# Performance work log

Hardware: AMD Instinct MI355X
Metric: run time of the kernel (lower is better)

The kernel has to match this reference:

```python
import jax, jax.numpy as jnp
import numpy as np

B, N, L = 1, 128, 256
D_MSA, D_HID, D_PAIR = 256, 32, 128
EPS = 1e-5


def setup_inputs() -> dict:
    key = jax.random.key(0)
    ks = jax.random.split(key, 8)
    msa = jax.random.normal(ks[0], (B, N, L, D_MSA), dtype=jnp.float32)
    pair = jax.random.normal(ks[1], (B, L, L, D_PAIR), dtype=jnp.float32)
    symmids = jax.random.randint(ks[2], (1,), 0, 1, dtype=jnp.int64)
    symmsub = jax.random.randint(ks[3], (1,), 0, 1, dtype=jnp.int64)
    # learned params (lecun-normal-ish scale = 1/sqrt(fan_in))
    ln_gamma = jnp.ones((D_MSA,), jnp.float32)
    ln_beta = jnp.zeros((D_MSA,), jnp.float32)
    w_left = jax.random.normal(ks[4], (D_MSA, D_HID), jnp.float32) / np.sqrt(D_MSA)
    b_left = jnp.zeros((D_HID,), jnp.float32)
    w_right = jax.random.normal(ks[5], (D_MSA, D_HID), jnp.float32) / np.sqrt(D_MSA)
    b_right = jnp.zeros((D_HID,), jnp.float32)
    w_out = jax.random.normal(ks[6], (D_HID * D_HID, D_PAIR), jnp.float32) / np.sqrt(D_HID * D_HID)
    b_out = jnp.zeros((D_PAIR,), jnp.float32)
    return {
        "msa": msa, "pair": pair, "symmids": symmids, "symmsub": symmsub,
        "ln_gamma": ln_gamma, "ln_beta": ln_beta,
        "w_left": w_left, "b_left": b_left,
        "w_right": w_right, "b_right": b_right,
        "w_out": w_out, "b_out": b_out,
    }


def reference(msa, pair, symmids, symmsub, ln_gamma, ln_beta,
              w_left, b_left, w_right, b_right, w_out, b_out):
    b, n, l, _ = msa.shape
    # LayerNorm over d_msa (biased variance, matching torch)
    mu = jnp.mean(msa, axis=-1, keepdims=True)
    var = jnp.mean(jnp.square(msa - mu), axis=-1, keepdims=True)
    x = (msa - mu) * jax.lax.rsqrt(var + EPS) * ln_gamma + ln_beta
    left = x @ w_left + b_left                       # [b, n, l, d_h]
    right = (x @ w_right + b_right) / float(n)       # [b, n, l, d_h]
    # outer product, reduced over MSA (s) dim -> [b, l, m, d_h, d_h]
    out = jnp.einsum('bsli,bsmj->blmij', left, right).reshape(b, l, l, -1)
    out = out @ w_out + b_out                        # [b, l, l, d_pair]
    return pair + out
```

## Files before the change

### kernel.cpp

```cpp
#include <hip/hip_runtime.h>


typedef float v4f __attribute__((ext_vector_type(4)));
typedef short v8s __attribute__((ext_vector_type(8)));

static __device__ inline unsigned short f2bf(float x) {
    unsigned int u = __builtin_bit_cast(unsigned int, x);
    return (unsigned short)((u + 0x7fffu + ((u >> 16) & 1u)) >> 16);
}

static __device__ inline void gl_lds16(const unsigned short* g, unsigned short* l) {
    __builtin_amdgcn_global_load_lds(
        (const __attribute__((address_space(1))) unsigned int*)g,
        (__attribute__((address_space(3))) unsigned int*)(unsigned long long)l,
        16, 0, 0);
}

__global__ __launch_bounds__(256) void k_prep(const float* __restrict__ w_out,
                                              const float* __restrict__ wl,
                                              const float* __restrict__ wr,
                                              unsigned short* __restrict__ w3,
                                              unsigned short* __restrict__ wB) {
    const int b = blockIdx.x, t = threadIdx.x;
    unsigned short tmp[8];
    if (b < 64) {
        int tgt = b * 2048 + t * 8;
        int lane6 = (tgt >> 3) & 63, quad = lane6 >> 4, l15 = lane6 & 15;
        int w = (tgt >> 9) & 3, tt = (tgt >> 11) & 1;
        int inner = (tgt >> 12) & 1, ck = tgt >> 13;
        int p = w * 32 + tt * 16 + l15;
        for (int e = 0; e < 8; ++e) {
            int kp = ck * 64 + inner * 32 + quad * 8 + e;
            int j1 = (kp >> 9) & 1, qd = (kp >> 7) & 3, lp = (kp >> 3) & 15;
            int i1 = (kp >> 2) & 1, r = kp & 3;
            int ii = i1 * 16 + qd * 4 + r, jj = j1 * 16 + lp;
            tmp[e] = f2bf(w_out[(ii * 32 + jj) * 128 + p]);
        }
        *(uint4*)&w3[tgt] = *(const uint4*)tmp;
    } else {
        int tgt = (b - 64) * 2048 + t * 8;
        int frag = tgt >> 9, lane6 = (tgt >> 3) & 63;
        int nt = frag >> 3, ks = frag & 7;
        int quad = lane6 >> 4, l15 = lane6 & 15;
        int c = nt * 16 + l15;
        const float* src = (c < 32) ? wl : wr;
        int cc = c & 31;
        for (int e = 0; e < 8; ++e) {
            int d = ks * 32 + quad * 8 + e;
            tmp[e] = f2bf(src[d * 32 + cc]);
        }
        *(uint4*)&wB[tgt] = *(const uint4*)tmp;
    }
}

__global__ __launch_bounds__(256) void k_lnproj(
    const float* __restrict__ msa, const float* __restrict__ gamma, const float* __restrict__ beta,
    const unsigned short* __restrict__ wB, const float* __restrict__ bl, const float* __restrict__ br,
    unsigned short* __restrict__ leftT, unsigned short* __restrict__ rightT) {
    __shared__ unsigned short xb[32 * 264];
    __shared__ unsigned short outT[64 * 40];

    const int t = threadIdx.x, lane = t & 63, w = t >> 6;
    const int l = blockIdx.x, s0 = blockIdx.y * 32;
    const int quad = lane >> 4, l15 = lane & 15;

    float4 g4 = *(const float4*)&gamma[lane * 4];
    float4 be4 = *(const float4*)&beta[lane * 4];
    float4 vr[8]; float s1[8], s2[8];
    for (int r = 0; r < 8; ++r) {
        const float* row = msa + (size_t)((s0 + w * 8 + r) * 256 + l) * 256;
        vr[r] = *(const float4*)&row[lane * 4];
    }
    for (int r = 0; r < 8; ++r) {
        float4 v = vr[r];
        s1[r] = v.x + v.y + v.z + v.w;
        s2[r] = v.x * v.x + v.y * v.y + v.z * v.z + v.w * v.w;
    }
    for (int o = 32; o > 0; o >>= 1)
        for (int r = 0; r < 8; ++r) { s1[r] += __shfl_xor(s1[r], o); s2[r] += __shfl_xor(s2[r], o); }
    for (int r = 0; r < 8; ++r) {
        float mu = s1[r] * (1.f / 256);
        float rs = rsqrtf(s2[r] * (1.f / 256) - mu * mu + 1e-5f);
        float4 v = vr[r];
        ushort4 xs;
        xs.x = f2bf((v.x - mu) * rs * g4.x + be4.x);
        xs.y = f2bf((v.y - mu) * rs * g4.y + be4.y);
        xs.z = f2bf((v.z - mu) * rs * g4.z + be4.z);
        xs.w = f2bf((v.w - mu) * rs * g4.w + be4.w);
        *(ushort4*)&xb[(w * 8 + r) * 264 + lane * 4] = xs;
    }
    __syncthreads();

    const int mt = w >> 1, ntb = (w & 1) * 2;
    v4f acc[2] = {};
    const int frow = (mt * 16 + l15) * 264;
    const unsigned short* wBp = wB + lane * 8;
#pragma unroll
    for (int ks = 0; ks < 8; ++ks) {
        v8s a = *(const v8s*)&xb[frow + ks * 32 + quad * 8];
        v8s b0 = *(const v8s*)&wBp[(ntb * 8 + ks) * 512];
        v8s b1 = *(const v8s*)&wBp[((ntb + 1) * 8 + ks) * 512];
        acc[0] = __builtin_amdgcn_mfma_f32_16x16x32_bf16(a, b0, acc[0], 0, 0, 0);
        acc[1] = __builtin_amdgcn_mfma_f32_16x16x32_bf16(a, b1, acc[1], 0, 0, 0);
    }

    for (int tn = 0; tn < 2; ++tn) {
        int c = (ntb + tn) * 16 + l15;
        float bias = c < 32 ? bl[c] : br[c - 32];
        float scale = c < 32 ? 1.f : (1.f / 128);
        for (int r = 0; r < 4; ++r)
            outT[c * 40 + mt * 16 + quad * 4 + r] = f2bf((acc[tn][r] + bias) * scale);
    }
    __syncthreads();

    {
        int c = t >> 2, q = t & 3;
        uint4 vv = *(const uint4*)&outT[c * 40 + q * 8];
        int cc = c & 31;
        unsigned short* base = (c < 32) ? leftT : rightT;
        unsigned short* dst = base + l * 4096 + blockIdx.y * 1024
                            + (cc >> 4) * 512 + q * 128 + (cc & 15) * 8;
        *(uint4*)dst = vv;
    }
}

__global__ __launch_bounds__(256, 3) void k_outer(
    const unsigned short* __restrict__ leftT, const unsigned short* __restrict__ rightT,
    const unsigned short* __restrict__ w2g, const float* __restrict__ bout,
    const float* __restrict__ pairIn, float* __restrict__ out) {
    __shared__ alignas(16) unsigned short smem[16384];
    unsigned short* Ah = smem;
    unsigned short* Bh = smem + 8192;
    unsigned short* Obuf = smem;

    const int t = threadIdx.x, lane = t & 63, w = t >> 6;
    const int l0 = blockIdx.x * 4, m0 = blockIdx.y * 4;
    const int wm = w & 1, wn = w >> 1;
    const int quad = lane >> 4, l15 = lane & 15;

    float pf[8];
#pragma unroll
    for (int tt = 0; tt < 2; ++tt)
#pragma unroll
        for (int r = 0; r < 4; ++r) {
            int pr = quad * 4 + r;
            int p = (w * 2 + tt) * 16 + l15;
            size_t idx = (size_t)((l0 + (pr >> 2)) * 256 + (m0 + (pr & 3))) * 128 + p;
            pf[tt * 4 + r] = pairIn[idx];
        }

    const unsigned short* Asrc = leftT + l0 * 4096;
    const unsigned short* Bsrc = rightT + m0 * 4096;

    v4f acc[4][4] = {};
    for (int kh = 0; kh < 2; ++kh) {
        if (kh) __syncthreads();
#pragma unroll
        for (int it = 0; it < 4; ++it) {
            int x = (it * 256 + t) * 8;
            gl_lds16(&Asrc[(x >> 11) * 4096 + kh * 2048 + (x & 2047)], &Ah[x]);
            gl_lds16(&Bsrc[(x >> 11) * 4096 + kh * 2048 + (x & 2047)], &Bh[x]);
        }
        __syncthreads();
#pragma unroll
        for (int kl = 0; kl < 2; ++kl) {
            v8s a[4], bb[4];
#pragma unroll
            for (int i = 0; i < 4; ++i)
                a[i] = *(const v8s*)&Ah[(wm * 2 + (i >> 1)) * 2048 + kl * 1024 + (i & 1) * 512 + lane * 8];
#pragma unroll
            for (int j = 0; j < 4; ++j)
                bb[j] = *(const v8s*)&Bh[(wn * 2 + (j >> 1)) * 2048 + kl * 1024 + (j & 1) * 512 + lane * 8];
#pragma unroll
            for (int i = 0; i < 4; ++i)
#pragma unroll
                for (int j = 0; j < 4; ++j)
                    acc[i][j] = __builtin_amdgcn_mfma_f32_16x16x32_bf16(a[i], bb[j], acc[i][j], 0, 0, 0);
        }
    }
    __syncthreads();

    const unsigned short* wsrc = w2g + w * 512 + lane * 8;
    v8s A0 = *(const v8s*)&wsrc[0];
    v8s A1 = *(const v8s*)&wsrc[2048];
    v8s A2 = *(const v8s*)&wsrc[4096];
    v8s A3 = *(const v8s*)&wsrc[6144];
    v8s B0 = *(const v8s*)&wsrc[8192];
    v8s B1 = *(const v8s*)&wsrc[8192 + 2048];
    v8s B2 = *(const v8s*)&wsrc[8192 + 4096];
    v8s B3 = *(const v8s*)&wsrc[8192 + 6144];

    for (int a2 = 0; a2 < 2; ++a2)
        for (int b2 = 0; b2 < 2; ++b2) {
            int P = (wm * 2 + a2) * 4 + wn * 2 + b2;
            for (int j1 = 0; j1 < 2; ++j1) {
                unsigned short tmp8[8];
                for (int i1 = 0; i1 < 2; ++i1)
                    for (int r = 0; r < 4; ++r)
                        tmp8[i1 * 4 + r] = f2bf(acc[a2 * 2 + i1][b2 * 2 + j1][r]);
                int pg = (j1 * 64 + lane) ^ (P & 7) ^ ((P & 8) << 3);
                *(uint4*)&Obuf[P * 1024 + pg * 8] = *(const uint4*)tmp8;
            }
        }
    __syncthreads();

    v4f aI0[2] = {}, aI1[2] = {};
#pragma unroll
    for (int ck = 0; ck < 16; ck += 2) {
        {
            int g = ck * 8 + quad;
            v8s a = *(const v8s*)&Obuf[l15 * 1024 + ((g ^ (l15 & 7) ^ ((l15 & 8) << 3)) << 3)];
            aI0[0] = __builtin_amdgcn_mfma_f32_16x16x32_bf16(a, A0, aI0[0], 0, 0, 0);
            aI0[1] = __builtin_amdgcn_mfma_f32_16x16x32_bf16(a, A1, aI0[1], 0, 0, 0);
            int g2 = ck * 8 + 4 + quad;
            v8s a2 = *(const v8s*)&Obuf[l15 * 1024 + ((g2 ^ (l15 & 7) ^ ((l15 & 8) << 3)) << 3)];
            aI1[0] = __builtin_amdgcn_mfma_f32_16x16x32_bf16(a2, A2, aI1[0], 0, 0, 0);
            aI1[1] = __builtin_amdgcn_mfma_f32_16x16x32_bf16(a2, A3, aI1[1], 0, 0, 0);
            if (ck + 2 < 16) {
                const unsigned short* nx = wsrc + (ck + 2) * 8192;
                A0 = *(const v8s*)&nx[0];
                A1 = *(const v8s*)&nx[2048];
                A2 = *(const v8s*)&nx[4096];
                A3 = *(const v8s*)&nx[6144];
            }
        }
        {
            int g = (ck + 1) * 8 + quad;
            v8s a = *(const v8s*)&Obuf[l15 * 1024 + ((g ^ (l15 & 7) ^ ((l15 & 8) << 3)) << 3)];
            aI0[0] = __builtin_amdgcn_mfma_f32_16x16x32_bf16(a, B0, aI0[0], 0, 0, 0);
            aI0[1] = __builtin_amdgcn_mfma_f32_16x16x32_bf16(a, B1, aI0[1], 0, 0, 0);
            int g2 = (ck + 1) * 8 + 4 + quad;
            v8s a2 = *(const v8s*)&Obuf[l15 * 1024 + ((g2 ^ (l15 & 7) ^ ((l15 & 8) << 3)) << 3)];
            aI1[0] = __builtin_amdgcn_mfma_f32_16x16x32_bf16(a2, B2, aI1[0], 0, 0, 0);
            aI1[1] = __builtin_amdgcn_mfma_f32_16x16x32_bf16(a2, B3, aI1[1], 0, 0, 0);
            if (ck + 3 < 16) {
                const unsigned short* nx = wsrc + (ck + 3) * 8192;
                B0 = *(const v8s*)&nx[0];
                B1 = *(const v8s*)&nx[2048];
                B2 = *(const v8s*)&nx[4096];
                B3 = *(const v8s*)&nx[6144];
            }
        }
    }

#pragma unroll
    for (int tt = 0; tt < 2; ++tt) {
        int p = (w * 2 + tt) * 16 + l15;
        float bo = bout[p];
        v4f acc2 = aI0[tt] + aI1[tt];
#pragma unroll
        for (int r = 0; r < 4; ++r) {
            int pr = quad * 4 + r;
            size_t idx = (size_t)((l0 + (pr >> 2)) * 256 + (m0 + (pr & 3))) * 128 + p;
            out[idx] = pf[tt * 4 + r] + bo + acc2[r];
        }
    }
}

extern "C" void kernel_launch(void* const* d_in, const int* in_sizes, int n_in,
                              void* d_out, int out_size, void* d_ws, size_t ws_size,
                              hipStream_t stream) {
    const float* msa   = (const float*)d_in[0];
    const float* pairI = (const float*)d_in[1];
    const float* gamma = (const float*)d_in[4];
    const float* beta  = (const float*)d_in[5];
    const float* wl    = (const float*)d_in[6];
    const float* bl    = (const float*)d_in[7];
    const float* wr    = (const float*)d_in[8];
    const float* br    = (const float*)d_in[9];
    const float* wout  = (const float*)d_in[10];
    const float* bout  = (const float*)d_in[11];
    float* out = (float*)d_out;

    unsigned short* leftT  = (unsigned short*)d_ws;
    unsigned short* rightT = leftT + 256 * 32 * 128;
    unsigned short* w3     = rightT + 256 * 32 * 128;
    unsigned short* wB     = w3 + 131072;

    k_prep<<<dim3(72), 256, 0, stream>>>(wout, wl, wr, w3, wB);
    k_lnproj<<<dim3(256, 4), 256, 0, stream>>>(msa, gamma, beta, wB, bl, br, leftT, rightT);
    k_outer<<<dim3(64, 64), 256, 0, stream>>>(leftT, rightT, w3, bout, pairI, out);
}
```

Before: 172.2 us.

## Enlarge outer-product tile to 8x4 pairs with 512-thread blocks

The k_outer block now covers 8 l rows by 4 m columns with 8 waves instead of 4x4 with 4 waves. Each wave owns 16 output channels and reuses every w_out fragment across two 16-pair row groups, which halves the per-block weight loads per output and lets the right operand be shared by more rows. The w_out pre-layout in k_prep is changed to match the new wave-to-channel mapping. The pair input prefetch also moves later, after the first GEMM. The cost is doubled LDS per block (64 KB) and a bigger register budget, which may reduce occupancy.

After: 178.3 us. +3.5%, slower.

```diff
diff --git a/kernel.cpp b/kernel.cpp
--- a/kernel.cpp
+++ b/kernel.cpp
@@ -26,9 +26,9 @@
     if (b < 64) {
         int tgt = b * 2048 + t * 8;
         int lane6 = (tgt >> 3) & 63, quad = lane6 >> 4, l15 = lane6 & 15;
-        int w = (tgt >> 9) & 3, tt = (tgt >> 11) & 1;
+        int w = (tgt >> 9) & 7;
         int inner = (tgt >> 12) & 1, ck = tgt >> 13;
-        int p = w * 32 + tt * 16 + l15;
+        int p = w * 16 + l15;
         for (int e = 0; e < 8; ++e) {
             int kp = ck * 64 + inner * 32 + quad * 8 + e;
             int j1 = (kp >> 9) & 1, qd = (kp >> 7) & 3, lp = (kp >> 3) & 15;
@@ -124,30 +124,19 @@
     }
 }
 
-__global__ __launch_bounds__(256, 3) void k_outer(
+__global__ __launch_bounds__(512, 4) void k_outer(
     const unsigned short* __restrict__ leftT, const unsigned short* __restrict__ rightT,
     const unsigned short* __restrict__ w2g, const float* __restrict__ bout,
     const float* __restrict__ pairIn, float* __restrict__ out) {
-    __shared__ alignas(16) unsigned short smem[16384];
+    __shared__ alignas(16) unsigned short smem[32768];
     unsigned short* Ah = smem;
-    unsigned short* Bh = smem + 8192;
+    unsigned short* Bh = smem + 16384;
     unsigned short* Obuf = smem;
 
     const int t = threadIdx.x, lane = t & 63, w = t >> 6;
-    const int l0 = blockIdx.x * 4, m0 = blockIdx.y * 4;
-    const int wm = w & 1, wn = w >> 1;
+    const int l0 = blockIdx.x * 8, m0 = blockIdx.y * 4;
+    const int wm = w & 3, wn = w >> 2;
     const int quad = lane >> 4, l15 = lane & 15;
-
-    float pf[8];
-#pragma unroll
-    for (int tt = 0; tt < 2; ++tt)
-#pragma unroll
-        for (int r = 0; r < 4; ++r) {
-            int pr = quad * 4 + r;
-            int p = (w * 2 + tt) * 16 + l15;
-            size_t idx = (size_t)((l0 + (pr >> 2)) * 256 + (m0 + (pr & 3))) * 128 + p;
-            pf[tt * 4 + r] = pairIn[idx];
-        }
 
     const unsigned short* Asrc = leftT + l0 * 4096;
     const unsigned short* Bsrc = rightT + m0 * 4096;
@@ -157,8 +146,12 @@
         if (kh) __syncthreads();
 #pragma unroll
         for (int it = 0; it < 4; ++it) {
-            int x = (it * 256 + t) * 8;
+            int x = (it * 512 + t) * 8;
             gl_lds16(&Asrc[(x >> 11) * 4096 + kh * 2048 + (x & 2047)], &Ah[x]);
+        }
+#pragma unroll
+        for (int it = 0; it < 2; ++it) {
+            int x = (it * 512 + t) * 8;
             gl_lds16(&Bsrc[(x >> 11) * 4096 + kh * 2048 + (x & 2047)], &Bh[x]);
         }
         __syncthreads();
@@ -182,13 +175,19 @@
 
     const unsigned short* wsrc = w2g + w * 512 + lane * 8;
     v8s A0 = *(const v8s*)&wsrc[0];
-    v8s A1 = *(const v8s*)&wsrc[2048];
-    v8s A2 = *(const v8s*)&wsrc[4096];
-    v8s A3 = *(const v8s*)&wsrc[6144];
+    v8s A1 = *(const v8s*)&wsrc[4096];
     v8s B0 = *(const v8s*)&wsrc[8192];
-    v8s B1 = *(const v8s*)&wsrc[8192 + 2048];
-    v8s B2 = *(const v8s*)&wsrc[8192 + 4096];
-    v8s B3 = *(const v8s*)&wsrc[8192 + 6144];
+    v8s B1 = *(const v8s*)&wsrc[8192 + 4096];
+    const int p = w * 16 + l15;
+    float bo = bout[p];
+    float pf[8];
+#pragma unroll
+    for (int pm = 0; pm < 2; ++pm)
+#pragma unroll
+        for (int r = 0; r < 4; ++r) {
+            int P = pm * 16 + quad * 4 + r;
+            pf[pm * 4 + r] = pairIn[(size_t)((l0 + (P >> 2)) * 256 + (m0 + (P & 3))) * 128 + p];
+        }
 
     for (int a2 = 0; a2 < 2; ++a2)
         for (int b2 = 0; b2 < 2; ++b2) {
@@ -209,52 +208,52 @@
     for (int ck = 0; ck < 16; ck += 2) {
         {
             int g = ck * 8 + quad;
-            v8s a = *(const v8s*)&Obuf[l15 * 1024 + ((g ^ (l15 & 7) ^ ((l15 & 8) << 3)) << 3)];
-            aI0[0] = __builtin_amdgcn_mfma_f32_16x16x32_bf16(a, A0, aI0[0], 0, 0, 0);
-            aI0[1] = __builtin_amdgcn_mfma_f32_16x16x32_bf16(a, A1, aI0[1], 0, 0, 0);
+            int ch = ((g ^ (l15 & 7) ^ ((l15 & 8) << 3)) << 3);
+            v8s a0 = *(const v8s*)&Obuf[l15 * 1024 + ch];
+            v8s a1 = *(const v8s*)&Obuf[(16 + l15) * 1024 + ch];
+            aI0[0] = __builtin_amdgcn_mfma_f32_16x16x32_bf16(a0, A0, aI0[0], 0, 0, 0);
+            aI0[1] = __builtin_amdgcn_mfma_f32_16x16x32_bf16(a1, A0, aI0[1], 0, 0, 0);
             int g2 = ck * 8 + 4 + quad;
-            v8s a2 = *(const v8s*)&Obuf[l15 * 1024 + ((g2 ^ (l15 & 7) ^ ((l15 & 8) << 3)) << 3)];
-            aI1[0] = __builtin_amdgcn_mfma_f32_16x16x32_bf16(a2, A2, aI1[0], 0, 0, 0);
-            aI1[1] = __builtin_amdgcn_mfma_f32_16x16x32_bf16(a2, A3, aI1[1], 0, 0, 0);
+            int ch2 = ((g2 ^ (l15 & 7) ^ ((l15 & 8) << 3)) << 3);
+            v8s b0 = *(const v8s*)&Obuf[l15 * 1024 + ch2];
+            v8s b1 = *(const v8s*)&Obuf[(16 + l15) * 1024 + ch2];
+            aI1[0] = __builtin_amdgcn_mfma_f32_16x16x32_bf16(b0, A1, aI1[0], 0, 0, 0);
+            aI1[1] = __builtin_amdgcn_mfma_f32_16x16x32_bf16(b1, A1, aI1[1], 0, 0, 0);
             if (ck + 2 < 16) {
                 const unsigned short* nx = wsrc + (ck + 2) * 8192;
                 A0 = *(const v8s*)&nx[0];
-                A1 = *(const v8s*)&nx[2048];
-                A2 = *(const v8s*)&nx[4096];
-                A3 = *(const v8s*)&nx[6144];
+                A1 = *(const v8s*)&nx[4096];
             }
         }
         {
             int g = (ck + 1) * 8 + quad;
-            v8s a = *(const v8s*)&Obuf[l15 * 1024 + ((g ^ (l15 & 7) ^ ((l15 & 8) << 3)) << 3)];
-            aI0[0] = __builtin_amdgcn_mfma_f32_16x16x32_bf16(a, B0, aI0[0], 0, 0, 0);
-            aI0[1] = __builtin_amdgcn_mfma_f32_16x16x32_bf16(a, B1, aI0[1], 0, 0, 0);
+            int ch = ((g ^ (l15 & 7) ^ ((l15 & 8) << 3)) << 3);
+            v8s a0 = *(const v8s*)&Obuf[l15 * 1024 + ch];
+            v8s a1 = *(const v8s*)&Obuf[(16 + l15) * 1024 + ch];
+            aI0[0] = __builtin_amdgcn_mfma_f32_16x16x32_bf16(a0, B0, aI0[0], 0, 0, 0);
+            aI0[1] = __builtin_amdgcn_mfma_f32_16x16x32_bf16(a1, B0, aI0[1], 0, 0, 0);
             int g2 = (ck + 1) * 8 + 4 + quad;
-            v8s a2 = *(const v8s*)&Obuf[l15 * 1024 + ((g2 ^ (l15 & 7) ^ ((l15 & 8) << 3)) << 3)];
-            aI1[0] = __builtin_amdgcn_mfma_f32_16x16x32_bf16(a2, B2, aI1[0], 0, 0, 0);
-            aI1[1] = __builtin_amdgcn_mfma_f32_16x16x32_bf16(a2, B3, aI1[1], 0, 0, 0);
+            int ch2 = ((g2 ^ (l15 & 7) ^ ((l15 & 8) << 3)) << 3);
+            v8s b0 = *(const v8s*)&Obuf[l15 * 1024 + ch2];
+            v8s b1 = *(const v8s*)&Obuf[(16 + l15) * 1024 + ch2];
+            aI1[0] = __builtin_amdgcn_mfma_f32_16x16x32_bf16(b0, B1, aI1[0], 0, 0, 0);
+            aI1[1] = __builtin_amdgcn_mfma_f32_16x16x32_bf16(b1, B1, aI1[1], 0, 0, 0);
             if (ck + 3 < 16) {
                 const unsigned short* nx = wsrc + (ck + 3) * 8192;
                 B0 = *(const v8s*)&nx[0];
-                B1 = *(const v8s*)&nx[2048];
-                B2 = *(const v8s*)&nx[4096];
-                B3 = *(const v8s*)&nx[6144];
+                B1 = *(const v8s*)&nx[4096];
             }
         }
     }
 
 #pragma unroll
-    for (int tt = 0; tt < 2; ++tt) {
-        int p = (w * 2 + tt) * 16 + l15;
-        float bo = bout[p];
-        v4f acc2 = aI0[tt] + aI1[tt];
+    for (int pm = 0; pm < 2; ++pm)
 #pragma unroll
         for (int r = 0; r < 4; ++r) {
-            int pr = quad * 4 + r;
-            size_t idx = (size_t)((l0 + (pr >> 2)) * 256 + (m0 + (pr & 3))) * 128 + p;
-            out[idx] = pf[tt * 4 + r] + bo + acc2[r];
-        }
-    }
+            int P = pm * 16 + quad * 4 + r;
+            size_t idx = (size_t)((l0 + (P >> 2)) * 256 + (m0 + (P & 3))) * 128 + p;
+            out[idx] = pf[pm * 4 + r] + bo + aI0[pm][r] + aI1[pm][r];
+        }
 }
 
 extern "C" void kernel_launch(void* const* d_in, const int* in_sizes, int n_in,
@@ -279,5 +278,5 @@
 
     k_prep<<<dim3(72), 256, 0, stream>>>(wout, wl, wr, w3, wB);
     k_lnproj<<<dim3(256, 4), 256, 0, stream>>>(msa, gamma, beta, wB, bl, br, leftT, rightT);
-    k_outer<<<dim3(64, 64), 256, 0, stream>>>(leftT, rightT, w3, bout, pairI, out);
-}
+    k_outer<<<dim3(32, 64), 512, 0, stream>>>(leftT, rightT, w3, bout, pairI, out);
+}
```
